# Kernel optimization log

Hardware: AMD Instinct MI355X
Metric: run time of the kernel (lower is better)

Reference implementation:

```python
import jax, jax.numpy as jnp
import numpy as np

B = 4096      # batch rows
D = 2048      # feature dim (all matrices square D x D)
NNZ = 16384


def setup_inputs() -> dict:
    key = jax.random.key(0)
    ks = jax.random.split(key, 12)
    inp = {"x": jax.random.normal(ks[0], (B, D), dtype=jnp.float32)}
    for i in range(3):
        inp[f"rows{i}"] = jax.random.randint(ks[1 + 3 * i], (NNZ,), 0, D, dtype=jnp.int32)
        inp[f"cols{i}"] = jax.random.randint(ks[2 + 3 * i], (NNZ,), 0, D, dtype=jnp.int32)
        inp[f"vals{i}"] = jax.random.normal(ks[3 + 3 * i], (NNZ,), dtype=jnp.float32)
    inp["bias"] = jax.random.normal(ks[10], (D,), dtype=jnp.float32)
    return inp


def _spmm_t(res, rows, cols, vals, out_dim):
    """Compute res @ M^T with M given in COO (rows, cols, vals), shape (out_dim, in_dim).
    Equivalent to transpose(sparse.mm(M, res^T)). Duplicate indices sum (COO semantics)."""
    contrib = res[:, cols] * vals  # (B, nnz) gather + scale
    return jnp.zeros((res.shape[0], out_dim), res.dtype).at[:, rows].add(contrib)


def reference(x, rows0, cols0, vals0, rows1, cols1, vals1, rows2, cols2, vals2, bias):
    squeeze = x.ndim == 1
    res = x[None, :] if squeeze else x
    # torch loop iterates reversed(range(len(mats))): matrix 2 first, then 1, then 0
    for rows, cols, vals in ((rows2, cols2, vals2), (rows1, cols1, vals1), (rows0, cols0, vals0)):
        res = _spmm_t(res, rows, cols, vals, D)
    res = res + bias
    return res[0] if squeeze else res
```

## Files before the change

### kernel.cpp

```cpp
#include <hip/hip_runtime.h>


#define BATCH 4096
#define DIM   2048
#define NNZc  16384
#define NT    256
#define BCAP  40

typedef short bf16x8 __attribute__((ext_vector_type(8)));
typedef float f32x4  __attribute__((ext_vector_type(4)));

__device__ __forceinline__ unsigned short f2bf(float f) {
    unsigned u = __float_as_uint(f);
    unsigned r = (u + 0x7fffu + ((u >> 16) & 1u)) >> 16;
    return (unsigned short)r;
}

__device__ __forceinline__ void gload16(const void* g, void* l) {
    __builtin_amdgcn_global_load_lds((const __attribute__((address_space(1))) void*)g,
                                     (__attribute__((address_space(3))) void*)l, 16, 0, 0);
}

__global__ void zero_kernel(int* __restrict__ p) {
    int i = blockIdx.x * NT + threadIdx.x;
    if (i < 3 * DIM) p[i] = 0;
}

__global__ void scatterd_kernel(const int* __restrict__ rows0, const int* __restrict__ cols0,
                                const float* __restrict__ vals0,
                                const int* __restrict__ rows1, const int* __restrict__ cols1,
                                const float* __restrict__ vals1,
                                const int* __restrict__ rows2, const int* __restrict__ cols2,
                                const float* __restrict__ vals2,
                                int* __restrict__ cnt,
                                int* __restrict__ colB, float* __restrict__ valB) {
    int e = blockIdx.x * NT + threadIdx.x;
    int m = e >> 14, i = e & (NNZc - 1);
    const int*   rp = (m == 0) ? rows0 : (m == 1) ? rows1 : rows2;
    const int*   cp = (m == 0) ? cols0 : (m == 1) ? cols1 : cols2;
    const float* vp = (m == 0) ? vals0 : (m == 1) ? vals1 : vals2;
    int r = rp[i];
    int slot = atomicAdd(&cnt[m * DIM + r], 1);
    if (slot < BCAP) {
        colB[(m * DIM + r) * BCAP + slot] = cp[i];
        valB[(m * DIM + r) * BCAP + slot] = vp[i];
    }
}

#define RPB  2
#define PCAP 2048
__global__ __launch_bounds__(NT) void mcxconv_kernel(
        const float* __restrict__ x, unsigned short* __restrict__ Xb,
        const int* __restrict__ cnt, const int* __restrict__ colB,
        const float* __restrict__ valB, unsigned short* __restrict__ Mc) {
    #pragma unroll
    for (int u = 0; u < 4; ++u) {
        size_t i = (((size_t)blockIdx.x * 4 + u) * NT + threadIdx.x) * 8;
        float4 a = *(const float4*)(x + i);
        float4 b = *(const float4*)(x + i + 4);
        unsigned short o[8] = {f2bf(a.x), f2bf(a.y), f2bf(a.z), f2bf(a.w),
                               f2bf(b.x), f2bf(b.y), f2bf(b.z), f2bf(b.w)};
        *(ulonglong2*)(Xb + i) = *(ulonglong2*)o;
    }

    __shared__ float acc[RPB * DIM];
    __shared__ int   pk[PCAP];
    __shared__ float pw[PCAP];
    __shared__ int   npairs;

    const int tid = threadIdx.x;
    const int r0  = blockIdx.x * RPB;

    f32x4* az = (f32x4*)acc;
    #pragma unroll
    for (int j = tid; j < RPB * DIM / 4; j += NT) az[j] = (f32x4){0.f, 0.f, 0.f, 0.f};
    if (tid == 0) npairs = 0;
    __syncthreads();

    #pragma unroll
    for (int k = 0; k < RPB; ++k) {
        int row = r0 + k;
        int n0 = min(cnt[row], BCAP);
        for (int i = tid; i < n0; i += NT) {
            int   c0 = colB[row * BCAP + i];
            float v0 = valB[row * BCAP + i];
            int n1 = min(cnt[DIM + c0], BCAP);
            for (int j = 0; j < n1; ++j) {
                float w  = v0 * valB[(DIM + c0) * BCAP + j];
                int   c1 = colB[(DIM + c0) * BCAP + j];
                int slot = atomicAdd(&npairs, 1);
                if (slot < PCAP) { pk[slot] = (k << 16) | c1; pw[slot] = w; }
                else {
                    int n2 = min(cnt[2 * DIM + c1], BCAP);
                    for (int q = 0; q < n2; ++q)
                        atomicAdd(&acc[k * DIM + colB[(2 * DIM + c1) * BCAP + q]],
                                  w * valB[(2 * DIM + c1) * BCAP + q]);
                }
            }
        }
    }
    __syncthreads();

    int np = min(npairs, PCAP);
    for (int p = tid; p < np; p += NT) {
        int   k  = pk[p] >> 16, c1 = pk[p] & 0xffff;
        float w  = pw[p];
        int n2 = min(cnt[2 * DIM + c1], BCAP);
        const int*   cb = colB + (2 * DIM + c1) * BCAP;
        const float* vb = valB + (2 * DIM + c1) * BCAP;
        for (int q = 0; q < n2; ++q)
            atomicAdd(&acc[k * DIM + cb[q]], w * vb[q]);
    }
    __syncthreads();

    #pragma unroll
    for (int k = 0; k < RPB; ++k) {
        unsigned short o[8];
        #pragma unroll
        for (int jj = 0; jj < 8; ++jj) o[jj] = f2bf(acc[k * DIM + tid * 8 + jj]);
        *(ulonglong2*)(Mc + (size_t)(r0 + k) * DIM + tid * 8) = *(ulonglong2*)o;
    }
}

#define BM 128
#define BN 256
#define BK 64
#define NS (DIM / BK)
#define A_SL (BM * BK * 2)
#define B_SL (BN * BK * 2)
#define SLOT (A_SL + B_SL)
#define GEMM_LDS (3 * SLOT)

__global__ __launch_bounds__(512, 2) void gemm8(
        const unsigned short* __restrict__ A,
        const unsigned short* __restrict__ Bm,
        const float* __restrict__ bias,
        float* __restrict__ C) {
    extern __shared__ char smem[];
    const int tid = threadIdx.x;
    const int l = tid & 63, w = tid >> 6;
    const int wm = w & 1, wn = w >> 1;

    const int bid = blockIdx.x;
    const int k = bid & 7, c = bid >> 3;
    const int tileM = ((k >> 1) * 8 + (c >> 2)) * BM;
    const int tileN = ((k & 1) * 4 + (c & 3)) * BN;

    const int r8   = l >> 3;
    const int clog = (l & 7) ^ r8;
    const unsigned short* aS0 = A  + (size_t)(tileM + 8 * w + r8) * DIM + clog * 8;
    const unsigned short* aS1 = aS0 + (size_t)64 * DIM;
    const unsigned short* bS0 = Bm + (size_t)(tileN + 32 * w + r8) * DIM + clog * 8;

#define STAGE(z, s) do {                                                   \
    gload16(aS0 +                (size_t)(s) * BK, (z) + w * 1024);        \
    gload16(aS1 +                (size_t)(s) * BK, (z) + 8192 + w * 1024); \
    gload16(bS0 +                (size_t)(s) * BK, (z) + A_SL + w * 4096);        \
    gload16(bS0 +  8 * DIM +     (size_t)(s) * BK, (z) + A_SL + w * 4096 + 1024); \
    gload16(bS0 + 16 * DIM +     (size_t)(s) * BK, (z) + A_SL + w * 4096 + 2048); \
    gload16(bS0 + 24 * DIM +     (size_t)(s) * BK, (z) + A_SL + w * 4096 + 3072); \
} while (0)

    const int rbyte = (l & 15) * 128;
    const int c0 = (((l >> 4)    ) ^ (l & 7)) * 16;
    const int c1 = (((l >> 4) + 4) ^ (l & 7)) * 16;

#define LOADFRAGS(z, A0, A1, B0, B1) do {                            \
    const char* _ab = (z) + wm * 8192 + rbyte;                       \
    A0[0] = *(const bf16x8*)(_ab + 0 * 2048 + c0);                   \
    A1[0] = *(const bf16x8*)(_ab + 0 * 2048 + c1);                   \
    A0[1] = *(const bf16x8*)(_ab + 1 * 2048 + c0);                   \
    A1[1] = *(const bf16x8*)(_ab + 1 * 2048 + c1);                   \
    A0[2] = *(const bf16x8*)(_ab + 2 * 2048 + c0);                   \
    A1[2] = *(const bf16x8*)(_ab + 2 * 2048 + c1);                   \
    A0[3] = *(const bf16x8*)(_ab + 3 * 2048 + c0);                   \
    A1[3] = *(const bf16x8*)(_ab + 3 * 2048 + c1);                   \
    const char* _bb = (z) + A_SL + wn * 8192 + rbyte;                \
    B0[0] = *(const bf16x8*)(_bb + 0 * 2048 + c0);                   \
    B1[0] = *(const bf16x8*)(_bb + 0 * 2048 + c1);                   \
    B0[1] = *(const bf16x8*)(_bb + 1 * 2048 + c0);                   \
    B1[1] = *(const bf16x8*)(_bb + 1 * 2048 + c1);                   \
    B0[2] = *(const bf16x8*)(_bb + 2 * 2048 + c0);                   \
    B1[2] = *(const bf16x8*)(_bb + 2 * 2048 + c1);                   \
    B0[3] = *(const bf16x8*)(_bb + 3 * 2048 + c0);                   \
    B1[3] = *(const bf16x8*)(_bb + 3 * 2048 + c1);                   \
} while (0)

#define PIN(X) asm volatile("" : "+v"(X[0]), "+v"(X[1]), "+v"(X[2]), "+v"(X[3]))

#define MFMA32(A0, A1, B0, B1) do {                                                    \
    _Pragma("unroll")                                                                  \
    for (int _q = 0; _q < 4; ++_q)                                                     \
        _Pragma("unroll")                                                              \
        for (int _j = 0; _j < 4; ++_j) {                                               \
            acc[_q][_j] = __builtin_amdgcn_mfma_f32_16x16x32_bf16(A0[_q], B0[_j],      \
                                                                  acc[_q][_j], 0,0,0); \
            acc[_q][_j] = __builtin_amdgcn_mfma_f32_16x16x32_bf16(A1[_q], B1[_j],      \
                                                                  acc[_q][_j], 0,0,0); \
        }                                                                              \
} while (0)

    bf16x8 Ae0[4], Ae1[4], Be0[4], Be1[4];
    bf16x8 Ao0[4], Ao1[4], Bo0[4], Bo1[4];
    f32x4 acc[4][4] = {};

    char* p0 = smem;
    char* p1 = smem + SLOT;
    char* p2 = smem + 2 * SLOT;

    STAGE(p0, 0);
    STAGE(p1, 1);
    asm volatile("s_waitcnt vmcnt(6)" ::: "memory");
    __builtin_amdgcn_sched_barrier(0);
    __builtin_amdgcn_s_barrier();
    LOADFRAGS(p0, Ae0, Ae1, Be0, Be1);
    PIN(Ae0); PIN(Ae1); PIN(Be0); PIN(Be1);
    asm volatile("s_waitcnt lgkmcnt(0)" ::: "memory");
    __builtin_amdgcn_sched_barrier(0);

#define BODY(CURA0, CURA1, CURB0, CURB1, NXTA0, NXTA1, NXTB0, NXTB1, S) do {  \
    STAGE(p2, (S) + 2);                                                        \
    __builtin_amdgcn_sched_barrier(0);                                         \
    asm volatile("s_waitcnt vmcnt(6)" ::: "memory");                           \
    __builtin_amdgcn_sched_barrier(0);                                         \
    __builtin_amdgcn_s_barrier();                                              \
    LOADFRAGS(p1, NXTA0, NXTA1, NXTB0, NXTB1);                                 \
    PIN(NXTA0); PIN(NXTA1); PIN(NXTB0); PIN(NXTB1);                            \
    __builtin_amdgcn_sched_barrier(0);                                         \
    __builtin_amdgcn_s_setprio(1);                                             \
    MFMA32(CURA0, CURA1, CURB0, CURB1);                                        \
    __builtin_amdgcn_s_setprio(0);                                             \
    asm volatile("s_waitcnt lgkmcnt(0)" ::: "memory");                         \
    __builtin_amdgcn_sched_barrier(0);                                         \
    { char* _t = p0; p0 = p1; p1 = p2; p2 = _t; }                              \
} while (0)

    for (int t = 0; t < 15; ++t) {
        const int s = 2 * t;
        BODY(Ae0, Ae1, Be0, Be1, Ao0, Ao1, Bo0, Bo1, s);
        BODY(Ao0, Ao1, Bo0, Bo1, Ae0, Ae1, Be0, Be1, s + 1);
    }
    asm volatile("s_waitcnt vmcnt(0)" ::: "memory");
    __builtin_amdgcn_sched_barrier(0);
    __builtin_amdgcn_s_barrier();
    LOADFRAGS(p1, Ao0, Ao1, Bo0, Bo1);
    PIN(Ao0); PIN(Ao1); PIN(Bo0); PIN(Bo1);
    __builtin_amdgcn_sched_barrier(0);
    __builtin_amdgcn_s_setprio(1);
    MFMA32(Ae0, Ae1, Be0, Be1);
    __builtin_amdgcn_s_setprio(0);
    asm volatile("s_waitcnt lgkmcnt(0)" ::: "memory");
    __builtin_amdgcn_sched_barrier(0);
    MFMA32(Ao0, Ao1, Bo0, Bo1);

    #pragma unroll
    for (int j = 0; j < 4; ++j) {
        int col = tileN + wn * 64 + j * 16 + (l & 15);
        float bj = bias[col];
        #pragma unroll
        for (int i = 0; i < 4; ++i) {
            int rw = tileM + wm * 64 + i * 16 + (l >> 4) * 4;
            #pragma unroll
            for (int r = 0; r < 4; ++r)
                C[(size_t)(rw + r) * DIM + col] = acc[i][j][r] + bj;
        }
    }
}

extern "C" void kernel_launch(void* const* d_in, const int* in_sizes, int n_in,
                              void* d_out, int out_size, void* d_ws, size_t ws_size,
                              hipStream_t stream) {
    const float* x     = (const float*)d_in[0];
    const int*   rows0 = (const int*)  d_in[1];
    const int*   cols0 = (const int*)  d_in[2];
    const float* vals0 = (const float*)d_in[3];
    const int*   rows1 = (const int*)  d_in[4];
    const int*   cols1 = (const int*)  d_in[5];
    const float* vals1 = (const float*)d_in[6];
    const int*   rows2 = (const int*)  d_in[7];
    const int*   cols2 = (const int*)  d_in[8];
    const float* vals2 = (const float*)d_in[9];
    const float* bias  = (const float*)d_in[10];
    float* out = (float*)d_out;

    char* ws = (char*)d_ws;
    unsigned short* Mc = (unsigned short*)ws;
    unsigned short* Xb = (unsigned short*)(ws + 8388608);
    int*   cnt  = (int*)(ws + 25165824);
    int*   colB = cnt + 3 * DIM;
    float* valB = (float*)(colB + 3 * DIM * BCAP);

    zero_kernel<<<(3 * DIM + NT - 1) / NT, NT, 0, stream>>>(cnt);
    scatterd_kernel<<<3 * NNZc / NT, NT, 0, stream>>>(rows0, cols0, vals0,
                                                      rows1, cols1, vals1,
                                                      rows2, cols2, vals2,
                                                      cnt, colB, valB);
    mcxconv_kernel<<<DIM / RPB, NT, 0, stream>>>(x, Xb, cnt, colB, valB, Mc);

    (void)hipFuncSetAttribute((const void*)gemm8,
                              hipFuncAttributeMaxDynamicSharedMemorySize, GEMM_LDS);
    gemm8<<<256, 512, GEMM_LDS, stream>>>(Xb, Mc, bias, out);
}
```

Baseline: 70.03 us.

## Pack COO buckets as int2 and parallelize second-level expansion across 16 lanes

Stores bucket column and value interleaved as int2 so each entry takes one 8-byte load instead of two separate loads. In the matrix-product precompute, the first-level row entries are staged in shared memory and each 16-thread group takes one entry, spreading its second-level neighbors across lanes. Before, each thread walked a full second-level bucket serially and only about n0 threads did any work. The change adds a __syncthreads per row and relies on the bucket capacity of 40 fitting within the 256 threads.

```diff
diff --git a/kernel.cpp b/kernel.cpp
--- a/kernel.cpp
+++ b/kernel.cpp
@@ -32,8 +32,7 @@
                                 const float* __restrict__ vals1,
                                 const int* __restrict__ rows2, const int* __restrict__ cols2,
                                 const float* __restrict__ vals2,
-                                int* __restrict__ cnt,
-                                int* __restrict__ colB, float* __restrict__ valB) {
+                                int* __restrict__ cnt, int2* __restrict__ bkt) {
     int e = blockIdx.x * NT + threadIdx.x;
     int m = e >> 14, i = e & (NNZc - 1);
     const int*   rp = (m == 0) ? rows0 : (m == 1) ? rows1 : rows2;
@@ -41,18 +40,16 @@
     const float* vp = (m == 0) ? vals0 : (m == 1) ? vals1 : vals2;
     int r = rp[i];
     int slot = atomicAdd(&cnt[m * DIM + r], 1);
-    if (slot < BCAP) {
-        colB[(m * DIM + r) * BCAP + slot] = cp[i];
-        valB[(m * DIM + r) * BCAP + slot] = vp[i];
-    }
+    if (slot < BCAP)
+        bkt[(m * DIM + r) * BCAP + slot] = make_int2(cp[i], __float_as_int(vp[i]));
 }
 
 #define RPB  2
 #define PCAP 2048
 __global__ __launch_bounds__(NT) void mcxconv_kernel(
         const float* __restrict__ x, unsigned short* __restrict__ Xb,
-        const int* __restrict__ cnt, const int* __restrict__ colB,
-        const float* __restrict__ valB, unsigned short* __restrict__ Mc) {
+        const int* __restrict__ cnt, const int2* __restrict__ bkt,
+        unsigned short* __restrict__ Mc) {
     #pragma unroll
     for (int u = 0; u < 4; ++u) {
         size_t i = (((size_t)blockIdx.x * 4 + u) * NT + threadIdx.x) * 8;
@@ -66,6 +63,8 @@
     __shared__ float acc[RPB * DIM];
     __shared__ int   pk[PCAP];
     __shared__ float pw[PCAP];
+    __shared__ int   sc0[BCAP];
+    __shared__ float sv0[BCAP];
     __shared__ int   npairs;
 
     const int tid = threadIdx.x;
@@ -77,39 +76,51 @@
     if (tid == 0) npairs = 0;
     __syncthreads();
 
+    const int i0 = tid >> 4, jj = tid & 15;
     #pragma unroll
     for (int k = 0; k < RPB; ++k) {
         int row = r0 + k;
         int n0 = min(cnt[row], BCAP);
-        for (int i = tid; i < n0; i += NT) {
-            int   c0 = colB[row * BCAP + i];
-            float v0 = valB[row * BCAP + i];
-            int n1 = min(cnt[DIM + c0], BCAP);
-            for (int j = 0; j < n1; ++j) {
-                float w  = v0 * valB[(DIM + c0) * BCAP + j];
-                int   c1 = colB[(DIM + c0) * BCAP + j];
-                int slot = atomicAdd(&npairs, 1);
-                if (slot < PCAP) { pk[slot] = (k << 16) | c1; pw[slot] = w; }
-                else {
-                    int n2 = min(cnt[2 * DIM + c1], BCAP);
-                    for (int q = 0; q < n2; ++q)
-                        atomicAdd(&acc[k * DIM + colB[(2 * DIM + c1) * BCAP + q]],
-                                  w * valB[(2 * DIM + c1) * BCAP + q]);
+        if (tid < n0) {
+            int2 e0 = bkt[row * BCAP + tid];
+            sc0[tid] = e0.x; sv0[tid] = __int_as_float(e0.y);
+        }
+        __syncthreads();
+        for (int ib = 0; ib < n0; ib += 16) {
+            int i = ib + i0;
+            if (i < n0) {
+                int   c0v = sc0[i];
+                float v0  = sv0[i];
+                int n1 = min(cnt[DIM + c0v], BCAP);
+                for (int j = jj; j < n1; j += 16) {
+                    int2  e1 = bkt[(DIM + c0v) * BCAP + j];
+                    float w  = v0 * __int_as_float(e1.y);
+                    int slot = atomicAdd(&npairs, 1);
+                    if (slot < PCAP) { pk[slot] = (k << 16) | e1.x; pw[slot] = w; }
+                    else {
+                        int n2 = min(cnt[2 * DIM + e1.x], BCAP);
+                        const int2* b2 = bkt + (2 * DIM + e1.x) * BCAP;
+                        for (int q = 0; q < n2; ++q) {
+                            int2 e2 = b2[q];
+                            atomicAdd(&acc[k * DIM + e2.x], w * __int_as_float(e2.y));
+                        }
+                    }
                 }
             }
         }
-    }
-    __syncthreads();
+        __syncthreads();
+    }
 
     int np = min(npairs, PCAP);
     for (int p = tid; p < np; p += NT) {
         int   k  = pk[p] >> 16, c1 = pk[p] & 0xffff;
         float w  = pw[p];
         int n2 = min(cnt[2 * DIM + c1], BCAP);
-        const int*   cb = colB + (2 * DIM + c1) * BCAP;
-        const float* vb = valB + (2 * DIM + c1) * BCAP;
-        for (int q = 0; q < n2; ++q)
-            atomicAdd(&acc[k * DIM + cb[q]], w * vb[q]);
+        const int2* b2 = bkt + (2 * DIM + c1) * BCAP;
+        for (int q = 0; q < n2; ++q) {
+            int2 e2 = b2[q];
+            atomicAdd(&acc[k * DIM + e2.x], w * __int_as_float(e2.y));
+        }
     }
     __syncthreads();
 
@@ -117,7 +128,7 @@
     for (int k = 0; k < RPB; ++k) {
         unsigned short o[8];
         #pragma unroll
-        for (int jj = 0; jj < 8; ++jj) o[jj] = f2bf(acc[k * DIM + tid * 8 + jj]);
+        for (int jj2 = 0; jj2 < 8; ++jj2) o[jj2] = f2bf(acc[k * DIM + tid * 8 + jj2]);
         *(ulonglong2*)(Mc + (size_t)(r0 + k) * DIM + tid * 8) = *(ulonglong2*)o;
     }
 }
@@ -286,16 +297,15 @@
     char* ws = (char*)d_ws;
     unsigned short* Mc = (unsigned short*)ws;
     unsigned short* Xb = (unsigned short*)(ws + 8388608);
-    int*   cnt  = (int*)(ws + 25165824);
-    int*   colB = cnt + 3 * DIM;
-    float* valB = (float*)(colB + 3 * DIM * BCAP);
+    int*  cnt = (int*)(ws + 25165824);
+    int2* bkt = (int2*)(cnt + 3 * DIM);
 
     zero_kernel<<<(3 * DIM + NT - 1) / NT, NT, 0, stream>>>(cnt);
     scatterd_kernel<<<3 * NNZc / NT, NT, 0, stream>>>(rows0, cols0, vals0,
                                                       rows1, cols1, vals1,
                                                       rows2, cols2, vals2,
-                                                      cnt, colB, valB);
-    mcxconv_kernel<<<DIM / RPB, NT, 0, stream>>>(x, Xb, cnt, colB, valB, Mc);
+                                                      cnt, bkt);
+    mcxconv_kernel<<<DIM / RPB, NT, 0, stream>>>(x, Xb, cnt, bkt, Mc);
 
     (void)hipFuncSetAttribute((const void*)gemm8,
                               hipFuncAttributeMaxDynamicSharedMemorySize, GEMM_LDS);
```

Measured after the change: 64.70 us. 7.6% less time.
